# Kernel optimization log

Measured on AMD Instinct MI355X. Metric: run time of the kernel, lower is better.

Reference implementation:

```python
import jax, jax.numpy as jnp
import numpy as np

N_NODES = 100000


def setup_inputs() -> dict:
    key = jax.random.key(0)
    k1, k2, k3 = jax.random.split(key, 3)
    x = jax.random.normal(k1, (N_NODES, 128), dtype=jnp.float32)
    edge_index = jax.random.randint(k2, (2, 1600000), 0, N_NODES, dtype=jnp.int32)
    # GCNConv linear weight: [out_features, in_features], bias: [out_features]
    W = jax.random.normal(k3, (128, 128), dtype=jnp.float32) * (1.0 / np.sqrt(128.0))
    b = jnp.zeros((128,), dtype=jnp.float32)
    return {"x": x, "edge_index": edge_index, "W": W, "b": b}


def reference(x, edge_index, W, b):
    n = x.shape[0]
    # --- add self loops (PyG GCNConv default) ---
    loop = jnp.arange(n, dtype=edge_index.dtype)
    row = jnp.concatenate([edge_index[0], loop])  # source nodes
    col = jnp.concatenate([edge_index[1], loop])  # target nodes
    # --- symmetric degree normalization D^{-1/2} A_hat D^{-1/2} ---
    ones = jnp.ones(row.shape[0], dtype=x.dtype)
    deg = jax.ops.segment_sum(ones, col, num_segments=n)
    deg_inv_sqrt = jnp.where(deg > 0, jax.lax.rsqrt(deg), 0.0)
    norm = deg_inv_sqrt[row] * deg_inv_sqrt[col]  # [E + N]
    # --- linear transform then gather-normalize-scatter aggregation ---
    xw = x @ W.T  # [N, out]
    msgs = xw[row] * norm[:, None]  # [E + N, out]
    out = jax.ops.segment_sum(msgs, col, num_segments=n)  # [N, out]
    return out + b
```

## Files before the change

kernel.cpp:

```cpp
#include <hip/hip_runtime.h>

#define NF 128
#define WLD2 136

#define BSHIFT 7
#define BNODES (1 << BSHIFT)
#define NBUCK 782
#define BCAP 2560
#define CHUNK 4096

typedef __attribute__((ext_vector_type(8))) short bf16x8;
typedef __attribute__((ext_vector_type(4))) float f32x4;

__device__ inline short f2bf_rne(float f) {
    unsigned u = __float_as_uint(f);
    u += 0x7FFFu + ((u >> 16) & 1u);
    return (short)(u >> 16);
}
__device__ inline float bf_lo(unsigned u) { return __uint_as_float(u << 16); }
__device__ inline float bf_hi(unsigned u) { return __uint_as_float(u & 0xFFFF0000u); }

__global__ void binit_kernel(int* __restrict__ bcursor) {
    int i = blockIdx.x * blockDim.x + threadIdx.x;
    if (i < NBUCK) bcursor[i] = i * BCAP;
}

__global__ __launch_bounds__(256) void bucketize_kernel(const int* __restrict__ row,
                                                        const int* __restrict__ col,
                                                        int* __restrict__ bcursor,
                                                        int2* __restrict__ bpairs, int E) {
    __shared__ int hist[NBUCK];
    __shared__ int base[NBUCK];
    const int t = threadIdx.x;
    const int e0 = blockIdx.x * CHUNK;
    const int cnt = min(CHUNK, E - e0);
    for (int i = t; i < NBUCK; i += 256) hist[i] = 0;
    __syncthreads();
    for (int i = t; i < cnt; i += 256) {
        atomicAdd(&hist[col[e0 + i] >> BSHIFT], 1);
    }
    __syncthreads();
    for (int i = t; i < NBUCK; i += 256) {
        int h = hist[i];
        base[i] = h ? atomicAdd(&bcursor[i], h) : 0;
        hist[i] = 0;
    }
    __syncthreads();
    for (int i = t; i < cnt; i += 256) {
        int c = col[e0 + i];
        int r = row[e0 + i];
        int bk = c >> BSHIFT;
        int pos = base[bk] + atomicAdd(&hist[bk], 1);
        bpairs[pos] = make_int2(c, r);
    }
}

__device__ inline int block_exclusive_scan_256(int val) {
    __shared__ int wsum[4];
    int lane = threadIdx.x & 63, wave = threadIdx.x >> 6;
    int x = val;
#pragma unroll
    for (int off = 1; off < 64; off <<= 1) {
        int y = __shfl_up(x, off, 64);
        if (lane >= off) x += y;
    }
    if (lane == 63) wsum[wave] = x;
    __syncthreads();
    if (threadIdx.x == 0) {
        int acc = 0;
        for (int w = 0; w < 4; ++w) { int t = wsum[w]; wsum[w] = acc; acc += t; }
    }
    __syncthreads();
    return x - val + wsum[wave];
}

__global__ __launch_bounds__(256) void bucket_build_kernel(const int2* __restrict__ bpairs,
                                                           const int* __restrict__ bcursor,
                                                           int* __restrict__ cnt,
                                                           float* __restrict__ dis,
                                                           int* __restrict__ offs,
                                                           int* __restrict__ ed, int N) {
    __shared__ int2 pe[BCAP];
    __shared__ int h[BNODES];
    __shared__ int edl[BCAP];
    const int b = blockIdx.x;
    const int node0 = b << BSHIFT;
    const int nn = min(BNODES, N - node0);
    const int start = b * BCAP;
    const int ecnt = bcursor[b] - start;
    for (int i = threadIdx.x; i < nn; i += 256) h[i] = 0;
    __syncthreads();
    for (int i = threadIdx.x; i < ecnt; i += 256) {
        int2 p = bpairs[start + i];
        p.x -= node0;
        pe[i] = p;
        atomicAdd(&h[p.x], 1);
    }
    __syncthreads();
    const int t = threadIdx.x;
    int v0 = (2 * t < nn) ? h[2 * t] : 0;
    int v1 = (2 * t + 1 < nn) ? h[2 * t + 1] : 0;
    int exc = block_exclusive_scan_256(v0 + v1);
    if (2 * t < nn) {
        offs[node0 + 2 * t] = start + exc;
        cnt[node0 + 2 * t] = v0;
        dis[node0 + 2 * t] = rsqrtf((float)v0 + 1.0f);
        h[2 * t] = exc;
    }
    if (2 * t + 1 < nn) {
        offs[node0 + 2 * t + 1] = start + exc + v0;
        cnt[node0 + 2 * t + 1] = v1;
        dis[node0 + 2 * t + 1] = rsqrtf((float)v1 + 1.0f);
        h[2 * t + 1] = exc + v0;
    }
    __syncthreads();
    for (int i = threadIdx.x; i < ecnt; i += 256) {
        int2 p = pe[i];
        int pos = atomicAdd(&h[p.x], 1);
        edl[pos] = p.y;
    }
    __syncthreads();
    for (int i = threadIdx.x; i < ecnt; i += 256) ed[start + i] = edl[i];
}

__global__ __launch_bounds__(256) void gemm_xws_kernel(const float* __restrict__ x,
                                                       const float* __restrict__ W,
                                                       const float* __restrict__ dis,
                                                       unsigned short* __restrict__ xws,
                                                       int n) {
    __shared__ short Wl[NF * WLD2];

    for (int idx = threadIdx.x; idx < NF * 32; idx += 256) {
        int o = idx >> 5;
        int kq = (idx & 31) << 2;
        float4 v = *(const float4*)(W + o * NF + kq);
        short* d = &Wl[o * WLD2 + kq];
        d[0] = f2bf_rne(v.x); d[1] = f2bf_rne(v.y);
        d[2] = f2bf_rne(v.z); d[3] = f2bf_rne(v.w);
    }
    __syncthreads();

    const int lane = threadIdx.x & 63;
    const int wave = threadIdx.x >> 6;
    const int mbase = wave * 32;
    const int l15 = lane & 15;
    const int quad = lane >> 4;
    const int tile = blockIdx.x * 128;

    f32x4 acc[2][8];
#pragma unroll
    for (int mb = 0; mb < 2; ++mb)
#pragma unroll
        for (int nb = 0; nb < 8; ++nb) acc[mb][nb] = (f32x4)0.0f;

#pragma unroll
    for (int kc = 0; kc < 4; ++kc) {
        const int kof = kc * 32 + quad * 8;
        bf16x8 Bf[8];
#pragma unroll
        for (int nb = 0; nb < 8; ++nb) {
            int o = nb * 16 + l15;
            Bf[nb] = *(const bf16x8*)(&Wl[o * WLD2 + kof]);
        }
#pragma unroll
        for (int mb = 0; mb < 2; ++mb) {
            int r = tile + mbase + mb * 16 + l15;
            if (r >= n) r = n - 1;
            const float4* ap = (const float4*)(x + (size_t)r * NF + kof);
            float4 a0 = ap[0], a1 = ap[1];
            bf16x8 Af;
            Af[0] = f2bf_rne(a0.x); Af[1] = f2bf_rne(a0.y);
            Af[2] = f2bf_rne(a0.z); Af[3] = f2bf_rne(a0.w);
            Af[4] = f2bf_rne(a1.x); Af[5] = f2bf_rne(a1.y);
            Af[6] = f2bf_rne(a1.z); Af[7] = f2bf_rne(a1.w);
#pragma unroll
            for (int nb = 0; nb < 8; ++nb)
                acc[mb][nb] = __builtin_amdgcn_mfma_f32_16x16x32_bf16(Af, Bf[nb], acc[mb][nb], 0, 0, 0);
        }
    }

#pragma unroll
    for (int mb = 0; mb < 2; ++mb) {
        int rbase = tile + mbase + mb * 16 + quad * 4;
#pragma unroll
        for (int reg = 0; reg < 4; ++reg) {
            int r = rbase + reg;
            if (r < n) {
                float dsc = dis[r];
#pragma unroll
                for (int nb = 0; nb < 8; ++nb) {
                    int c = nb * 16 + l15;
                    xws[(size_t)r * NF + c] = (unsigned short)f2bf_rne(acc[mb][nb][reg] * dsc);
                }
            }
        }
    }
}

__global__ __launch_bounds__(256) void gather_kernel(const int* __restrict__ ed,
                                                     const int* __restrict__ offs,
                                                     const int* __restrict__ cnt,
                                                     const float* __restrict__ dis,
                                                     const unsigned short* __restrict__ xws,
                                                     const float* __restrict__ b,
                                                     float* __restrict__ out, int n) {
    int node = (int)((blockIdx.x * blockDim.x + threadIdx.x) >> 6);
    const int lane = threadIdx.x & 63;
    if (node >= n) return;
    node = __builtin_amdgcn_readfirstlane(node);
    const int lsub = lane & 31;
    const bool lo = lane < 32;
    const float dc = dis[node];
    const int start = offs[node];
    const int end = start + cnt[node];

    float ax = 0.f, ay = 0.f, az = 0.f, aw = 0.f;
    {
        uint2 u = *(const uint2*)(xws + (size_t)node * NF + lsub * 4);
        if (lo) { ax = bf_lo(u.x); ay = bf_hi(u.x); az = bf_lo(u.y); aw = bf_hi(u.y); }
    }
    int i = start;
    for (; i + 8 <= end; i += 8) {
        int r0 = ed[i], r1 = ed[i + 1], r2 = ed[i + 2], r3 = ed[i + 3];
        int r4 = ed[i + 4], r5 = ed[i + 5], r6 = ed[i + 6], r7 = ed[i + 7];
        int sa = lo ? r0 : r1, sb = lo ? r2 : r3, sc = lo ? r4 : r5, sd = lo ? r6 : r7;
        uint2 ua = *(const uint2*)(xws + (size_t)sa * NF + lsub * 4);
        uint2 ub = *(const uint2*)(xws + (size_t)sb * NF + lsub * 4);
        uint2 uc = *(const uint2*)(xws + (size_t)sc * NF + lsub * 4);
        uint2 ud = *(const uint2*)(xws + (size_t)sd * NF + lsub * 4);
        ax += bf_lo(ua.x) + bf_lo(ub.x) + bf_lo(uc.x) + bf_lo(ud.x);
        ay += bf_hi(ua.x) + bf_hi(ub.x) + bf_hi(uc.x) + bf_hi(ud.x);
        az += bf_lo(ua.y) + bf_lo(ub.y) + bf_lo(uc.y) + bf_lo(ud.y);
        aw += bf_hi(ua.y) + bf_hi(ub.y) + bf_hi(uc.y) + bf_hi(ud.y);
    }
    for (; i + 2 <= end; i += 2) {
        int r0 = ed[i], r1 = ed[i + 1];
        int s = lo ? r0 : r1;
        uint2 u = *(const uint2*)(xws + (size_t)s * NF + lsub * 4);
        ax += bf_lo(u.x); ay += bf_hi(u.x); az += bf_lo(u.y); aw += bf_hi(u.y);
    }
    if (i < end) {
        int r0 = ed[i];
        uint2 u = *(const uint2*)(xws + (size_t)r0 * NF + lsub * 4);
        if (lo) { ax += bf_lo(u.x); ay += bf_hi(u.x); az += bf_lo(u.y); aw += bf_hi(u.y); }
    }
    ax += __shfl_xor(ax, 32, 64);
    ay += __shfl_xor(ay, 32, 64);
    az += __shfl_xor(az, 32, 64);
    aw += __shfl_xor(aw, 32, 64);
    if (lo) {
        float4 bb = ((const float4*)b)[lsub];
        float4 o;
        o.x = fmaf(ax, dc, bb.x);
        o.y = fmaf(ay, dc, bb.y);
        o.z = fmaf(az, dc, bb.z);
        o.w = fmaf(aw, dc, bb.w);
        ((float4*)(out + (size_t)node * NF))[lsub] = o;
    }
}

extern "C" void kernel_launch(void* const* d_in, const int* in_sizes, int n_in,
                              void* d_out, int out_size, void* d_ws, size_t ws_size,
                              hipStream_t stream) {
    const float* x = (const float*)d_in[0];
    const int* ei = (const int*)d_in[1];
    const float* W = (const float*)d_in[2];
    const float* b = (const float*)d_in[3];
    float* out = (float*)d_out;

    const int N = in_sizes[0] / NF;
    const int E = in_sizes[1] / 2;
    const int* row = ei;
    const int* col = ei + E;

    char* ws = (char*)d_ws;
    unsigned short* xws = (unsigned short*)ws;
    ws += (size_t)N * NF * sizeof(unsigned short);
    int* cnt = (int*)ws; ws += (size_t)N * sizeof(int);
    float* dis = (float*)ws; ws += (size_t)N * sizeof(float);
    int* offs = (int*)ws; ws += (size_t)N * sizeof(int);
    int2* bpairs = (int2*)ws; ws += (size_t)NBUCK * BCAP * sizeof(int2);
    int* bcursor = (int*)ws; ws += 1024 * sizeof(int);
    int* ed = (int*)ws;

    const int CB = (E + CHUNK - 1) / CHUNK;

    binit_kernel<<<(NBUCK + 255) / 256, 256, 0, stream>>>(bcursor);
    bucketize_kernel<<<CB, 256, 0, stream>>>(row, col, bcursor, bpairs, E);

    bucket_build_kernel<<<NBUCK, 256, 0, stream>>>(bpairs, bcursor, cnt, dis, offs, ed, N);

    gemm_xws_kernel<<<(N + 127) / 128, 256, 0, stream>>>(x, W, dis, xws, N);

    {
        int nodes_per_block = 256 / 64;
        int blocks = (N + nodes_per_block - 1) / nodes_per_block;
        gather_kernel<<<blocks, 256, 0, stream>>>(ed, offs, cnt, dis, xws, b, out, N);
    }
}
```

Measured before the change: 228.7 us.

## Pack bucket pairs into one int, stage edges in LDS, unroll gather wider

Bucketize now loads each chunk's (col,row) into shared memory once instead of re-reading global memory, and writes one packed int per edge (row<<7 | local col) instead of an int2. This halves the bucket scratch traffic and the reads in bucket_build. The gather loop is unrolled to 16 edges per iteration for more memory-level parallelism, and the gather launch is split into two half-range launches. Packing assumes row<<7 fits in 31 bits, which holds for N=100000. The extra launch adds a small overhead.

```diff
diff --git a/kernel.cpp b/kernel.cpp
--- a/kernel.cpp
+++ b/kernel.cpp
@@ -28,7 +28,8 @@
 __global__ __launch_bounds__(256) void bucketize_kernel(const int* __restrict__ row,
                                                         const int* __restrict__ col,
                                                         int* __restrict__ bcursor,
-                                                        int2* __restrict__ bpairs, int E) {
+                                                        int* __restrict__ bpacked, int E) {
+    __shared__ int2 pe[CHUNK];
     __shared__ int hist[NBUCK];
     __shared__ int base[NBUCK];
     const int t = threadIdx.x;
@@ -37,7 +38,10 @@
     for (int i = t; i < NBUCK; i += 256) hist[i] = 0;
     __syncthreads();
     for (int i = t; i < cnt; i += 256) {
-        atomicAdd(&hist[col[e0 + i] >> BSHIFT], 1);
+        int c = col[e0 + i];
+        int r = row[e0 + i];
+        pe[i] = make_int2(c, r);
+        atomicAdd(&hist[c >> BSHIFT], 1);
     }
     __syncthreads();
     for (int i = t; i < NBUCK; i += 256) {
@@ -47,11 +51,10 @@
     }
     __syncthreads();
     for (int i = t; i < cnt; i += 256) {
-        int c = col[e0 + i];
-        int r = row[e0 + i];
-        int bk = c >> BSHIFT;
+        int2 p = pe[i];
+        int bk = p.x >> BSHIFT;
         int pos = base[bk] + atomicAdd(&hist[bk], 1);
-        bpairs[pos] = make_int2(c, r);
+        bpacked[pos] = (p.y << BSHIFT) | (p.x & (BNODES - 1));
     }
 }
 
@@ -74,13 +77,13 @@
     return x - val + wsum[wave];
 }
 
-__global__ __launch_bounds__(256) void bucket_build_kernel(const int2* __restrict__ bpairs,
+__global__ __launch_bounds__(256) void bucket_build_kernel(const int* __restrict__ bpacked,
                                                            const int* __restrict__ bcursor,
                                                            int* __restrict__ cnt,
                                                            float* __restrict__ dis,
                                                            int* __restrict__ offs,
                                                            int* __restrict__ ed, int N) {
-    __shared__ int2 pe[BCAP];
+    __shared__ int pe[BCAP];
     __shared__ int h[BNODES];
     __shared__ int edl[BCAP];
     const int b = blockIdx.x;
@@ -91,10 +94,9 @@
     for (int i = threadIdx.x; i < nn; i += 256) h[i] = 0;
     __syncthreads();
     for (int i = threadIdx.x; i < ecnt; i += 256) {
-        int2 p = bpairs[start + i];
-        p.x -= node0;
+        int p = bpacked[start + i];
         pe[i] = p;
-        atomicAdd(&h[p.x], 1);
+        atomicAdd(&h[p & (BNODES - 1)], 1);
     }
     __syncthreads();
     const int t = threadIdx.x;
@@ -115,9 +117,9 @@
     }
     __syncthreads();
     for (int i = threadIdx.x; i < ecnt; i += 256) {
-        int2 p = pe[i];
-        int pos = atomicAdd(&h[p.x], 1);
-        edl[pos] = p.y;
+        int p = pe[i];
+        int pos = atomicAdd(&h[p & (BNODES - 1)], 1);
+        edl[pos] = p >> BSHIFT;
     }
     __syncthreads();
     for (int i = threadIdx.x; i < ecnt; i += 256) ed[start + i] = edl[i];
@@ -203,10 +205,11 @@
                                                      const float* __restrict__ dis,
                                                      const unsigned short* __restrict__ xws,
                                                      const float* __restrict__ b,
-                                                     float* __restrict__ out, int n) {
-    int node = (int)((blockIdx.x * blockDim.x + threadIdx.x) >> 6);
+                                                     float* __restrict__ out,
+                                                     int nbase, int nend) {
+    int node = nbase + (int)((blockIdx.x * blockDim.x + threadIdx.x) >> 6);
     const int lane = threadIdx.x & 63;
-    if (node >= n) return;
+    if (node >= nend) return;
     node = __builtin_amdgcn_readfirstlane(node);
     const int lsub = lane & 31;
     const bool lo = lane < 32;
@@ -220,7 +223,31 @@
         if (lo) { ax = bf_lo(u.x); ay = bf_hi(u.x); az = bf_lo(u.y); aw = bf_hi(u.y); }
     }
     int i = start;
-    for (; i + 8 <= end; i += 8) {
+    for (; i + 16 <= end; i += 16) {
+        int r0 = ed[i], r1 = ed[i + 1], r2 = ed[i + 2], r3 = ed[i + 3];
+        int r4 = ed[i + 4], r5 = ed[i + 5], r6 = ed[i + 6], r7 = ed[i + 7];
+        int r8 = ed[i + 8], r9 = ed[i + 9], ra = ed[i + 10], rb = ed[i + 11];
+        int rc = ed[i + 12], rd = ed[i + 13], re = ed[i + 14], rf = ed[i + 15];
+        int sa = lo ? r0 : r1, sb = lo ? r2 : r3, sc = lo ? r4 : r5, sd = lo ? r6 : r7;
+        int se = lo ? r8 : r9, sf = lo ? ra : rb, sg = lo ? rc : rd, sh = lo ? re : rf;
+        uint2 ua = *(const uint2*)(xws + (size_t)sa * NF + lsub * 4);
+        uint2 ub = *(const uint2*)(xws + (size_t)sb * NF + lsub * 4);
+        uint2 uc = *(const uint2*)(xws + (size_t)sc * NF + lsub * 4);
+        uint2 ud = *(const uint2*)(xws + (size_t)sd * NF + lsub * 4);
+        uint2 ue = *(const uint2*)(xws + (size_t)se * NF + lsub * 4);
+        uint2 uf = *(const uint2*)(xws + (size_t)sf * NF + lsub * 4);
+        uint2 ug = *(const uint2*)(xws + (size_t)sg * NF + lsub * 4);
+        uint2 uh = *(const uint2*)(xws + (size_t)sh * NF + lsub * 4);
+        ax += bf_lo(ua.x) + bf_lo(ub.x) + bf_lo(uc.x) + bf_lo(ud.x);
+        ay += bf_hi(ua.x) + bf_hi(ub.x) + bf_hi(uc.x) + bf_hi(ud.x);
+        az += bf_lo(ua.y) + bf_lo(ub.y) + bf_lo(uc.y) + bf_lo(ud.y);
+        aw += bf_hi(ua.y) + bf_hi(ub.y) + bf_hi(uc.y) + bf_hi(ud.y);
+        ax += bf_lo(ue.x) + bf_lo(uf.x) + bf_lo(ug.x) + bf_lo(uh.x);
+        ay += bf_hi(ue.x) + bf_hi(uf.x) + bf_hi(ug.x) + bf_hi(uh.x);
+        az += bf_lo(ue.y) + bf_lo(uf.y) + bf_lo(ug.y) + bf_lo(uh.y);
+        aw += bf_hi(ue.y) + bf_hi(uf.y) + bf_hi(ug.y) + bf_hi(uh.y);
+    }
+    if (i + 8 <= end) {
         int r0 = ed[i], r1 = ed[i + 1], r2 = ed[i + 2], r3 = ed[i + 3];
         int r4 = ed[i + 4], r5 = ed[i + 5], r6 = ed[i + 6], r7 = ed[i + 7];
         int sa = lo ? r0 : r1, sb = lo ? r2 : r3, sc = lo ? r4 : r5, sd = lo ? r6 : r7;
@@ -232,6 +259,7 @@
         ay += bf_hi(ua.x) + bf_hi(ub.x) + bf_hi(uc.x) + bf_hi(ud.x);
         az += bf_lo(ua.y) + bf_lo(ub.y) + bf_lo(uc.y) + bf_lo(ud.y);
         aw += bf_hi(ua.y) + bf_hi(ub.y) + bf_hi(uc.y) + bf_hi(ud.y);
+        i += 8;
     }
     for (; i + 2 <= end; i += 2) {
         int r0 = ed[i], r1 = ed[i + 1];
@@ -279,22 +307,24 @@
     int* cnt = (int*)ws; ws += (size_t)N * sizeof(int);
     float* dis = (float*)ws; ws += (size_t)N * sizeof(float);
     int* offs = (int*)ws; ws += (size_t)N * sizeof(int);
-    int2* bpairs = (int2*)ws; ws += (size_t)NBUCK * BCAP * sizeof(int2);
+    int* bpacked = (int*)ws; ws += (size_t)NBUCK * BCAP * sizeof(int);
     int* bcursor = (int*)ws; ws += 1024 * sizeof(int);
     int* ed = (int*)ws;
 
     const int CB = (E + CHUNK - 1) / CHUNK;
 
     binit_kernel<<<(NBUCK + 255) / 256, 256, 0, stream>>>(bcursor);
-    bucketize_kernel<<<CB, 256, 0, stream>>>(row, col, bcursor, bpairs, E);
-
-    bucket_build_kernel<<<NBUCK, 256, 0, stream>>>(bpairs, bcursor, cnt, dis, offs, ed, N);
+    bucketize_kernel<<<CB, 256, 0, stream>>>(row, col, bcursor, bpacked, E);
+
+    bucket_build_kernel<<<NBUCK, 256, 0, stream>>>(bpacked, bcursor, cnt, dis, offs, ed, N);
 
     gemm_xws_kernel<<<(N + 127) / 128, 256, 0, stream>>>(x, W, dis, xws, N);
 
     {
-        int nodes_per_block = 256 / 64;
-        int blocks = (N + nodes_per_block - 1) / nodes_per_block;
-        gather_kernel<<<blocks, 256, 0, stream>>>(ed, offs, cnt, dis, xws, b, out, N);
-    }
-}
+        int half = (N / 2 + 3) & ~3;
+        int blocks1 = (half + 3) / 4;
+        int blocks2 = (N - half + 3) / 4;
+        gather_kernel<<<blocks1, 256, 0, stream>>>(ed, offs, cnt, dis, xws, b, out, 0, half);
+        gather_kernel<<<blocks2, 256, 0, stream>>>(ed, offs, cnt, dis, xws, b, out, half, N);
+    }
+}
```

Result: faster. 221.6 us (-3.1%).
